# Performance work log

Measured on AMD Instinct MI355X. Metric: run time of the kernel, lower is better.

The kernel has to match this reference:

```python
import jax, jax.numpy as jnp
import numpy as np

HEADS = 8
DIM_HEAD = 64


def setup_inputs() -> dict:
    key = jax.random.key(0)
    ks = jax.random.split(key, 10)
    B, NQ, NK, D, INNER = 4, 2048, 2048, 1024, HEADS * DIM_HEAD
    w_scale = 0.02
    return {
        "x": jax.random.normal(ks[0], (B, NQ, D), jnp.float32),
        "context": jax.random.normal(ks[1], (B, NK, D), jnp.float32),
        "wq": jax.random.normal(ks[2], (D, INNER), jnp.float32) * w_scale,
        "bq": jax.random.normal(ks[3], (INNER,), jnp.float32) * w_scale,
        "wk": jax.random.normal(ks[4], (D, INNER), jnp.float32) * w_scale,
        "bk": jax.random.normal(ks[5], (INNER,), jnp.float32) * w_scale,
        "wv": jax.random.normal(ks[6], (D, INNER), jnp.float32) * w_scale,
        "bv": jax.random.normal(ks[7], (INNER,), jnp.float32) * w_scale,
        "wo": jax.random.normal(ks[8], (INNER, D), jnp.float32) * w_scale,
        "bo": jax.random.normal(ks[9], (D,), jnp.float32) * w_scale,
    }


def _split_heads(t):
    # [b, n, h*d] -> [b, h, n, d]
    b, n, _ = t.shape
    return t.reshape(b, n, HEADS, DIM_HEAD).transpose(0, 2, 1, 3)


def reference(x, context, wq, bq, wk, bk, wv, bv, wo, bo):
    scale = DIM_HEAD ** -0.5
    q = _split_heads(x @ wq + bq)        # [b, h, nq, d]
    k = _split_heads(context @ wk + bk)  # [b, h, nk, d]
    v = _split_heads(context @ wv + bv)  # [b, h, nk, d]
    sim = jnp.einsum('bhid,bhjd->bhij', q, k) * scale  # full score matrix, as in original
    attn = jax.nn.softmax(sim, axis=-1)
    out = jnp.einsum('bhij,bhjd->bhid', attn, v)       # [b, h, nq, d]
    b, h, n, d = out.shape
    out = out.transpose(0, 2, 1, 3).reshape(b, n, h * d)
    return out @ wo + bo
```

## Files before the change

### kernel.cpp

```cpp
#include <hip/hip_runtime.h>
#include <hip/hip_bf16.h>

typedef __attribute__((ext_vector_type(8))) short short8;
typedef __attribute__((ext_vector_type(4))) float f32x4;

__device__ __forceinline__ short f2bf(float f) {
  union { float f; unsigned u; } x; x.f = f;
  unsigned r = x.u + 0x7fffu + ((x.u >> 16) & 1u);
  return (short)(r >> 16);
}

__device__ __forceinline__ void gload16(const short* g, short* l) {
  __builtin_amdgcn_global_load_lds(
      (const __attribute__((address_space(1))) unsigned*)g,
      (__attribute__((address_space(3))) unsigned*)l, 16, 0, 0);
}

__global__ void cast_bf16_kernel(const float* __restrict__ src,
                                 short* __restrict__ dst, int n) {
  int i = (blockIdx.x * 256 + threadIdx.x) * 4;
  if (i < n) {
    float4 f = *(const float4*)(src + i);
    union { short s[4]; uint2 u; } o;
    o.s[0] = f2bf(f.x); o.s[1] = f2bf(f.y);
    o.s[2] = f2bf(f.z); o.s[3] = f2bf(f.w);
    *(uint2*)(dst + i) = o.u;
  }
}

__global__ __launch_bounds__(256) void transpose_cast_kernel(
    const float* __restrict__ src, short* __restrict__ dst, int R, int C) {
  __shared__ short tile[64][72];
  int tpc = C >> 6;
  int bx = blockIdx.x % tpc, by = blockIdx.x / tpc;
  int r0 = by * 64, c0 = bx * 64;
  int tx = threadIdx.x & 15, ty = threadIdx.x >> 4;
#pragma unroll
  for (int i = 0; i < 4; i++) {
    int r = i * 16 + ty;
    float4 f = *(const float4*)(src + (size_t)(r0 + r) * C + c0 + tx * 4);
    union { short s[4]; uint2 u; } o;
    o.s[0] = f2bf(f.x); o.s[1] = f2bf(f.y);
    o.s[2] = f2bf(f.z); o.s[3] = f2bf(f.w);
    *(uint2*)&tile[r][tx * 4] = o.u;
  }
  __syncthreads();
#pragma unroll
  for (int i = 0; i < 4; i++) {
    int c = i * 16 + ty;
    union { short s[4]; uint2 u; } o;
#pragma unroll
    for (int k = 0; k < 4; k++) o.s[k] = tile[tx * 4 + k][c];
    *(uint2*)(dst + (size_t)(c0 + c) * R + r0 + tx * 4) = o.u;
  }
}

__device__ __forceinline__ void gemm_core(
    const short* __restrict__ A, const short* __restrict__ Bt, int K,
    int mblk, int nblk, short* sA, short* sB, f32x4 (&acc)[4][4]) {
  int tid = threadIdx.x;
  int lane = tid & 63, wave = tid >> 6;
  int quad = lane >> 4, l15 = lane & 15;
  int wm = (wave >> 1) * 64, wn = (wave & 1) * 64;
  int sub = lane >> 3, e8 = lane & 7;
  int swz = (e8 ^ sub) << 3;
  int s0 = (quad ^ (l15 & 7)) << 3;
  const short* Ag = A + (size_t)(mblk + 32 * wave + sub) * K + swz;
  const short* Bg = Bt + (size_t)(nblk + 32 * wave + sub) * K + swz;
  short* Al = sA + 4 * wave * 512;
  short* Bl = sB + 4 * wave * 512;

  for (int k0 = 0; k0 < K; k0 += 64) {
    __syncthreads();
#pragma unroll
    for (int t = 0; t < 4; t++) {
      gload16(Ag + (size_t)(8 * t) * K + k0, Al + t * 512);
      gload16(Bg + (size_t)(8 * t) * K + k0, Bl + t * 512);
    }
    __syncthreads();
#pragma unroll
    for (int h = 0; h < 2; h++) {
      int so = s0 ^ (h << 5);
      short8 af[4], bf[4];
#pragma unroll
      for (int mt = 0; mt < 4; mt++)
        af[mt] = *(const short8*)(&sA[(wm + mt * 16 + l15) * 64 + so]);
#pragma unroll
      for (int nt = 0; nt < 4; nt++)
        bf[nt] = *(const short8*)(&sB[(wn + nt * 16 + l15) * 64 + so]);
#pragma unroll
      for (int mt = 0; mt < 4; mt++)
#pragma unroll
        for (int nt = 0; nt < 4; nt++)
          acc[mt][nt] = __builtin_amdgcn_mfma_f32_16x16x32_bf16(
              af[mt], bf[nt], acc[mt][nt], 0, 0, 0);
    }
  }
}

__global__ __launch_bounds__(256) void gemm_qkv(
    const short* __restrict__ xb, const short* __restrict__ cb,
    const short* __restrict__ wqt, const short* __restrict__ wkt,
    const short* __restrict__ wvt,
    const float* __restrict__ bq, const float* __restrict__ bk,
    const float* __restrict__ bv,
    short* __restrict__ Qb, short* __restrict__ Kb, short* __restrict__ Vt) {
  __shared__ __align__(16) short sA[128 * 64];
  __shared__ __align__(16) short sB[128 * 64];
  int z = blockIdx.z;
  const short* A  = (z == 0) ? xb : cb;
  const short* Bt = (z == 0) ? wqt : (z == 1) ? wkt : wvt;
  const float* bias = (z == 0) ? bq : (z == 1) ? bk : bv;
  short* out = (z == 0) ? Qb : (z == 1) ? Kb : Vt;
  float scale = (z == 0) ? 0.18033688011112042f : 1.0f;
  int mblk = blockIdx.x * 128, nblk = blockIdx.y * 128;
  f32x4 acc[4][4] = {};
  gemm_core(A, Bt, 1024, mblk, nblk, sA, sB, acc);

  int lane = threadIdx.x & 63, wave = threadIdx.x >> 6;
  int quad = lane >> 4, l15 = lane & 15;
  int wm = (wave >> 1) * 64, wn = (wave & 1) * 64;
#pragma unroll
  for (int nt = 0; nt < 4; nt++) {
    int col = nblk + wn + nt * 16 + l15;
    float bias_v = bias[col];
    int h = col >> 6, dh = col & 63;
#pragma unroll
    for (int mt = 0; mt < 4; mt++)
#pragma unroll
      for (int r = 0; r < 4; r++) {
        int row = mblk + wm + mt * 16 + quad * 4 + r;
        float v = (acc[mt][nt][r] + bias_v) * scale;
        int b = row >> 11, n = row & 2047;
        size_t base = ((size_t)(b * 8 + h)) << 17;
        size_t idx = (z == 2) ? base + ((size_t)dh << 11) + n
                              : base + ((size_t)n << 6) + dh;
        out[idx] = f2bf(v);
      }
  }
}

__global__ __launch_bounds__(256) void gemm_out(
    const short* __restrict__ Ob, const short* __restrict__ wot,
    const float* __restrict__ bo, float* __restrict__ out) {
  __shared__ __align__(16) short sA[128 * 64];
  __shared__ __align__(16) short sB[128 * 64];
  int mblk = blockIdx.x * 128, nblk = blockIdx.y * 128;
  f32x4 acc[4][4] = {};
  gemm_core(Ob, wot, 512, mblk, nblk, sA, sB, acc);
  int lane = threadIdx.x & 63, wave = threadIdx.x >> 6;
  int quad = lane >> 4, l15 = lane & 15;
  int wm = (wave >> 1) * 64, wn = (wave & 1) * 64;
#pragma unroll
  for (int nt = 0; nt < 4; nt++) {
    int col = nblk + wn + nt * 16 + l15;
    float bias_v = bo[col];
#pragma unroll
    for (int mt = 0; mt < 4; mt++)
#pragma unroll
      for (int r = 0; r < 4; r++) {
        int row = mblk + wm + mt * 16 + quad * 4 + r;
        out[(size_t)row * 1024 + col] = acc[mt][nt][r] + bias_v;
      }
  }
}

__global__ __launch_bounds__(256, 4) void attn_kernel(
    const short* __restrict__ Qb, const short* __restrict__ Kb,
    const short* __restrict__ Vt, short* __restrict__ Ob) {
  __shared__ __align__(16) short sK[64 * 64];
  __shared__ __align__(16) short sV[64 * 64];
  __shared__ __align__(16) unsigned sP[4][640];
  int tid = threadIdx.x;
  int lane = tid & 63, wave = tid >> 6;
  int quad = lane >> 4, l15 = lane & 15;
  int bh = blockIdx.x & 31, qt = blockIdx.x >> 5;
  const short* Qp = Qb + ((size_t)bh << 17);
  const short* Kp = Kb + ((size_t)bh << 17);
  const short* Vp = Vt + ((size_t)bh << 17);
  int qrow0 = qt * 64 + wave * 16;
  short8 qf0 = *(const short8*)(Qp + (size_t)(qrow0 + l15) * 64 + quad * 8);
  short8 qf1 = *(const short8*)(Qp + (size_t)(qrow0 + l15) * 64 + 32 + quad * 8);

  int jk0 = 2 * wave, jk1 = 2 * wave + 1;
  int sub = lane >> 3;
  int e8  = lane & 7;
  int swz = (e8 ^ sub) << 3;
  const short* kg0 = Kp + (size_t)(8 * jk0 + sub) * 64 + e8 * 8;
  const short* kg1 = Kp + (size_t)(8 * jk1 + sub) * 64 + e8 * 8;
  short* kl0 = &sK[(8 * jk0 + sub) * 64 + swz];
  short* kl1 = &sK[(8 * jk1 + sub) * 64 + swz];
  const short* vg0 = Vp + (size_t)(8 * jk0 + sub) * 2048 + e8 * 8;
  const short* vg1 = Vp + (size_t)(8 * jk1 + sub) * 2048 + e8 * 8;
  short* vl0 = &sV[(8 * jk0 + sub) * 64 + swz];
  short* vl1 = &sV[(8 * jk1 + sub) * 64 + swz];

  int s0 = (quad ^ (l15 & 7)) << 3;
  int s1 = s0 ^ 32;

  f32x4 o[4] = {};
  float lsum = 0.f;
  unsigned* pw = &sP[wave][0];

  uint4 rk0 = *(const uint4*)kg0, rk1 = *(const uint4*)kg1;
  uint4 rv0 = *(const uint4*)vg0, rv1 = *(const uint4*)vg1;

  for (int it = 0; it < 32; ++it) {
    __syncthreads();
    *(uint4*)kl0 = rk0; *(uint4*)kl1 = rk1;
    *(uint4*)vl0 = rv0; *(uint4*)vl1 = rv1;
    if (it < 31) {
      int off = (it + 1) * 64;
      rk0 = *(const uint4*)(kg0 + (size_t)off * 64);
      rk1 = *(const uint4*)(kg1 + (size_t)off * 64);
      rv0 = *(const uint4*)(vg0 + off);
      rv1 = *(const uint4*)(vg1 + off);
    }
    __syncthreads();
    f32x4 st[4];
#pragma unroll
    for (int jt = 0; jt < 4; jt++) {
      short8 k0 = *(const short8*)(&sK[(jt * 16 + l15) * 64 + s0]);
      short8 k1 = *(const short8*)(&sK[(jt * 16 + l15) * 64 + s1]);
      f32x4 zz = {0.f, 0.f, 0.f, 0.f};
      zz = __builtin_amdgcn_mfma_f32_16x16x32_bf16(k0, qf0, zz, 0, 0, 0);
      st[jt] = __builtin_amdgcn_mfma_f32_16x16x32_bf16(k1, qf1, zz, 0, 0, 0);
    }
#pragma unroll
    for (int jt = 0; jt < 4; jt++) {
      float p0 = exp2f(st[jt][0]), p1 = exp2f(st[jt][1]);
      float p2 = exp2f(st[jt][2]), p3 = exp2f(st[jt][3]);
      lsum += (p0 + p1) + (p2 + p3);
      union { __hip_bfloat162 b; unsigned u; } a0, a1;
      a0.b = __float22bfloat162_rn(make_float2(p0, p1));
      a1.b = __float22bfloat162_rn(make_float2(p2, p3));
      int kpair = 8 * jt + 2 * quad;
      pw[(kpair + 0) * 20 + l15] = a0.u;
      pw[(kpair + 1) * 20 + l15] = a1.u;
    }
    union { unsigned u[4]; short8 s; } P0, P1;
#pragma unroll
    for (int c = 0; c < 4; c++) {
      P0.u[c] = pw[(4 * quad + c) * 20 + l15];
      P1.u[c] = pw[(16 + 4 * quad + c) * 20 + l15];
    }
#pragma unroll
    for (int nt = 0; nt < 4; nt++) {
      short8 v0 = *(const short8*)(&sV[(nt * 16 + l15) * 64 + s0]);
      short8 v1 = *(const short8*)(&sV[(nt * 16 + l15) * 64 + s1]);
      o[nt] = __builtin_amdgcn_mfma_f32_16x16x32_bf16(v0, P0.s, o[nt], 0, 0, 0);
      o[nt] = __builtin_amdgcn_mfma_f32_16x16x32_bf16(v1, P1.s, o[nt], 0, 0, 0);
    }
  }
  lsum += __shfl_xor(lsum, 16, 64);
  lsum += __shfl_xor(lsum, 32, 64);
  float inv = 1.0f / lsum;
  int b = bh >> 3, h = bh & 7;
  size_t rowbase = ((size_t)b * 2048 + qrow0 + l15) * 512 + h * 64 + quad * 4;
#pragma unroll
  for (int nt = 0; nt < 4; nt++) {
    union { short s[4]; uint2 u; } pk2;
#pragma unroll
    for (int r = 0; r < 4; r++) pk2.s[r] = f2bf(o[nt][r] * inv);
    *(uint2*)(Ob + rowbase + nt * 16) = pk2.u;
  }
}

extern "C" void kernel_launch(void* const* d_in, const int* in_sizes, int n_in,
                              void* d_out, int out_size, void* d_ws, size_t ws_size,
                              hipStream_t stream) {
  const float* x   = (const float*)d_in[0];
  const float* ctx = (const float*)d_in[1];
  const float* wq  = (const float*)d_in[2];
  const float* bq  = (const float*)d_in[3];
  const float* wk  = (const float*)d_in[4];
  const float* bk  = (const float*)d_in[5];
  const float* wv  = (const float*)d_in[6];
  const float* bv  = (const float*)d_in[7];
  const float* wo  = (const float*)d_in[8];
  const float* bo  = (const float*)d_in[9];
  float* out = (float*)d_out;
  char* ws = (char*)d_ws;

  short* xb  = (short*)(ws);
  short* cb  = (short*)(ws + (16ull << 20));
  short* wqt = (short*)(ws + (32ull << 20));
  short* wkt = (short*)(ws + (33ull << 20));
  short* wvt = (short*)(ws + (34ull << 20));
  short* wot = (short*)(ws + (35ull << 20));
  short* Qb  = (short*)(ws + (36ull << 20));
  short* Kb  = (short*)(ws + (44ull << 20));
  short* Vt  = (short*)(ws + (52ull << 20));
  short* Ob  = (short*)(ws + (60ull << 20));

  cast_bf16_kernel<<<8192, 256, 0, stream>>>(x, xb, 1 << 23);
  cast_bf16_kernel<<<8192, 256, 0, stream>>>(ctx, cb, 1 << 23);
  transpose_cast_kernel<<<128, 256, 0, stream>>>(wq, wqt, 1024, 512);
  transpose_cast_kernel<<<128, 256, 0, stream>>>(wk, wkt, 1024, 512);
  transpose_cast_kernel<<<128, 256, 0, stream>>>(wv, wvt, 1024, 512);
  transpose_cast_kernel<<<128, 256, 0, stream>>>(wo, wot, 512, 1024);
  gemm_qkv<<<dim3(64, 4, 3), 256, 0, stream>>>(xb, cb, wqt, wkt, wvt,
                                               bq, bk, bv, Qb, Kb, Vt);
  attn_kernel<<<1024, 256, 0, stream>>>(Qb, Kb, Vt, Ob);
  gemm_out<<<dim3(64, 8), 256, 0, stream>>>(Ob, wot, bo, out);
}
```

Before: 264.7 us.

## Double-buffer attention K/V, process two query groups per wave, fuse prep kernels

```diff
diff --git a/kernel.cpp b/kernel.cpp
--- a/kernel.cpp
+++ b/kernel.cpp
@@ -3,6 +3,7 @@
 
 typedef __attribute__((ext_vector_type(8))) short short8;
 typedef __attribute__((ext_vector_type(4))) float f32x4;
+typedef __attribute__((ext_vector_type(2))) unsigned uint2u;
 
 __device__ __forceinline__ short f2bf(float f) {
   union { float f; unsigned u; } x; x.f = f;
@@ -16,21 +17,29 @@
       (__attribute__((address_space(3))) unsigned*)l, 16, 0, 0);
 }
 
-__global__ void cast_bf16_kernel(const float* __restrict__ src,
-                                 short* __restrict__ dst, int n) {
+__global__ void cast2_bf16_kernel(const float* __restrict__ a,
+                                  const float* __restrict__ b,
+                                  short* __restrict__ dst) {
   int i = (blockIdx.x * 256 + threadIdx.x) * 4;
-  if (i < n) {
-    float4 f = *(const float4*)(src + i);
-    union { short s[4]; uint2 u; } o;
-    o.s[0] = f2bf(f.x); o.s[1] = f2bf(f.y);
-    o.s[2] = f2bf(f.z); o.s[3] = f2bf(f.w);
-    *(uint2*)(dst + i) = o.u;
-  }
-}
-
-__global__ __launch_bounds__(256) void transpose_cast_kernel(
-    const float* __restrict__ src, short* __restrict__ dst, int R, int C) {
+  const float* s = (i < (1 << 23)) ? a : b;
+  int j = i & ((1 << 23) - 1);
+  float4 f = *(const float4*)(s + j);
+  union { short s[4]; uint2 u; } o;
+  o.s[0] = f2bf(f.x); o.s[1] = f2bf(f.y);
+  o.s[2] = f2bf(f.z); o.s[3] = f2bf(f.w);
+  *(uint2*)(dst + i) = o.u;
+}
+
+__global__ __launch_bounds__(256) void transpose_cast4_kernel(
+    const float* __restrict__ wq, const float* __restrict__ wk,
+    const float* __restrict__ wv, const float* __restrict__ wo,
+    short* __restrict__ wqt, short* __restrict__ wkt,
+    short* __restrict__ wvt, short* __restrict__ wot) {
   __shared__ short tile[64][72];
+  int z = blockIdx.z;
+  const float* src = (z == 0) ? wq : (z == 1) ? wk : (z == 2) ? wv : wo;
+  short* dst = (z == 0) ? wqt : (z == 1) ? wkt : (z == 2) ? wvt : wot;
+  int R = (z < 3) ? 1024 : 512, C = (z < 3) ? 512 : 1024;
   int tpc = C >> 6;
   int bx = blockIdx.x % tpc, by = blockIdx.x / tpc;
   int r0 = by * 64, c0 = bx * 64;
@@ -165,12 +174,11 @@
   }
 }
 
-__global__ __launch_bounds__(256, 4) void attn_kernel(
+__global__ __launch_bounds__(256, 2) void attn_kernel(
     const short* __restrict__ Qb, const short* __restrict__ Kb,
     const short* __restrict__ Vt, short* __restrict__ Ob) {
-  __shared__ __align__(16) short sK[64 * 64];
-  __shared__ __align__(16) short sV[64 * 64];
-  __shared__ __align__(16) unsigned sP[4][640];
+  __shared__ __align__(16) short sK[2 * 64 * 64];
+  __shared__ __align__(16) short sV[2 * 64 * 64];
   int tid = threadIdx.x;
   int lane = tid & 63, wave = tid >> 6;
   int quad = lane >> 4, l15 = lane & 15;
@@ -178,9 +186,15 @@
   const short* Qp = Qb + ((size_t)bh << 17);
   const short* Kp = Kb + ((size_t)bh << 17);
   const short* Vp = Vt + ((size_t)bh << 17);
-  int qrow0 = qt * 64 + wave * 16;
-  short8 qf0 = *(const short8*)(Qp + (size_t)(qrow0 + l15) * 64 + quad * 8);
-  short8 qf1 = *(const short8*)(Qp + (size_t)(qrow0 + l15) * 64 + 32 + quad * 8);
+  int qrow0 = qt * 128 + wave * 32;
+
+  short8 qf[2][2];
+#pragma unroll
+  for (int g = 0; g < 2; g++) {
+    const short* qrow = Qp + (size_t)(qrow0 + g * 16 + l15) * 64;
+    qf[g][0] = *(const short8*)(qrow + quad * 8);
+    qf[g][1] = *(const short8*)(qrow + 32 + quad * 8);
+  }
 
   int jk0 = 2 * wave, jk1 = 2 * wave + 1;
   int sub = lane >> 3;
@@ -188,81 +202,102 @@
   int swz = (e8 ^ sub) << 3;
   const short* kg0 = Kp + (size_t)(8 * jk0 + sub) * 64 + e8 * 8;
   const short* kg1 = Kp + (size_t)(8 * jk1 + sub) * 64 + e8 * 8;
-  short* kl0 = &sK[(8 * jk0 + sub) * 64 + swz];
-  short* kl1 = &sK[(8 * jk1 + sub) * 64 + swz];
   const short* vg0 = Vp + (size_t)(8 * jk0 + sub) * 2048 + e8 * 8;
   const short* vg1 = Vp + (size_t)(8 * jk1 + sub) * 2048 + e8 * 8;
-  short* vl0 = &sV[(8 * jk0 + sub) * 64 + swz];
-  short* vl1 = &sV[(8 * jk1 + sub) * 64 + swz];
+  int kw0 = (8 * jk0 + sub) * 64 + swz;
+  int kw1 = (8 * jk1 + sub) * 64 + swz;
 
   int s0 = (quad ^ (l15 & 7)) << 3;
   int s1 = s0 ^ 32;
 
-  f32x4 o[4] = {};
-  float lsum = 0.f;
-  unsigned* pw = &sP[wave][0];
+  f32x4 o[2][4] = {};
+  float lsum[2] = {0.f, 0.f};
 
   uint4 rk0 = *(const uint4*)kg0, rk1 = *(const uint4*)kg1;
   uint4 rv0 = *(const uint4*)vg0, rv1 = *(const uint4*)vg1;
+  *(uint4*)(sK + kw0) = rk0; *(uint4*)(sK + kw1) = rk1;
+  *(uint4*)(sV + kw0) = rv0; *(uint4*)(sV + kw1) = rv1;
+  rk0 = *(const uint4*)(kg0 + 4096); rk1 = *(const uint4*)(kg1 + 4096);
+  rv0 = *(const uint4*)(vg0 + 64);   rv1 = *(const uint4*)(vg1 + 64);
+  __syncthreads();
 
   for (int it = 0; it < 32; ++it) {
-    __syncthreads();
-    *(uint4*)kl0 = rk0; *(uint4*)kl1 = rk1;
-    *(uint4*)vl0 = rv0; *(uint4*)vl1 = rv1;
+    const short* sKr = sK + (it & 1) * 4096;
+    const short* sVr = sV + (it & 1) * 4096;
     if (it < 31) {
-      int off = (it + 1) * 64;
-      rk0 = *(const uint4*)(kg0 + (size_t)off * 64);
-      rk1 = *(const uint4*)(kg1 + (size_t)off * 64);
-      rv0 = *(const uint4*)(vg0 + off);
-      rv1 = *(const uint4*)(vg1 + off);
-    }
-    __syncthreads();
-    f32x4 st[4];
+      short* sKw = sK + ((it & 1) ^ 1) * 4096;
+      short* sVw = sV + ((it & 1) ^ 1) * 4096;
+      *(uint4*)(sKw + kw0) = rk0; *(uint4*)(sKw + kw1) = rk1;
+      *(uint4*)(sVw + kw0) = rv0; *(uint4*)(sVw + kw1) = rv1;
+      if (it < 30) {
+        size_t ko = (size_t)(it + 2) * 4096, vo = (size_t)(it + 2) * 64;
+        rk0 = *(const uint4*)(kg0 + ko); rk1 = *(const uint4*)(kg1 + ko);
+        rv0 = *(const uint4*)(vg0 + vo); rv1 = *(const uint4*)(vg1 + vo);
+      }
+    }
+    unsigned xp[2][4][2];
 #pragma unroll
     for (int jt = 0; jt < 4; jt++) {
-      short8 k0 = *(const short8*)(&sK[(jt * 16 + l15) * 64 + s0]);
-      short8 k1 = *(const short8*)(&sK[(jt * 16 + l15) * 64 + s1]);
-      f32x4 zz = {0.f, 0.f, 0.f, 0.f};
-      zz = __builtin_amdgcn_mfma_f32_16x16x32_bf16(k0, qf0, zz, 0, 0, 0);
-      st[jt] = __builtin_amdgcn_mfma_f32_16x16x32_bf16(k1, qf1, zz, 0, 0, 0);
-    }
-#pragma unroll
-    for (int jt = 0; jt < 4; jt++) {
-      float p0 = exp2f(st[jt][0]), p1 = exp2f(st[jt][1]);
-      float p2 = exp2f(st[jt][2]), p3 = exp2f(st[jt][3]);
-      lsum += (p0 + p1) + (p2 + p3);
-      union { __hip_bfloat162 b; unsigned u; } a0, a1;
-      a0.b = __float22bfloat162_rn(make_float2(p0, p1));
-      a1.b = __float22bfloat162_rn(make_float2(p2, p3));
-      int kpair = 8 * jt + 2 * quad;
-      pw[(kpair + 0) * 20 + l15] = a0.u;
-      pw[(kpair + 1) * 20 + l15] = a1.u;
-    }
-    union { unsigned u[4]; short8 s; } P0, P1;
-#pragma unroll
-    for (int c = 0; c < 4; c++) {
-      P0.u[c] = pw[(4 * quad + c) * 20 + l15];
-      P1.u[c] = pw[(16 + 4 * quad + c) * 20 + l15];
+      short8 k0 = *(const short8*)(&sKr[(jt * 16 + l15) * 64 + s0]);
+      short8 k1 = *(const short8*)(&sKr[(jt * 16 + l15) * 64 + s1]);
+#pragma unroll
+      for (int g = 0; g < 2; g++) {
+        f32x4 zz = {0.f, 0.f, 0.f, 0.f};
+        zz = __builtin_amdgcn_mfma_f32_16x16x32_bf16(k0, qf[g][0], zz, 0, 0, 0);
+        f32x4 st = __builtin_amdgcn_mfma_f32_16x16x32_bf16(k1, qf[g][1], zz, 0, 0, 0);
+        float p0 = exp2f(st[0]), p1 = exp2f(st[1]);
+        float p2 = exp2f(st[2]), p3 = exp2f(st[3]);
+        lsum[g] += (p0 + p1) + (p2 + p3);
+        union { __hip_bfloat162 b; unsigned u; } a0, a1;
+        a0.b = __float22bfloat162_rn(make_float2(p0, p1));
+        a1.b = __float22bfloat162_rn(make_float2(p2, p3));
+        xp[g][jt][0] = a0.u; xp[g][jt][1] = a1.u;
+      }
+    }
+    short8 pf[2][2];
+#pragma unroll
+    for (int g = 0; g < 2; g++) {
+#pragma unroll
+      for (int hb = 0; hb < 2; hb++) {
+        unsigned x0 = xp[g][2 * hb][0], x1 = xp[g][2 * hb][1];
+        unsigned x2 = xp[g][2 * hb + 1][0], x3 = xp[g][2 * hb + 1][1];
+        uint2u r1 = __builtin_amdgcn_permlane32_swap(x0, x2, false, false);
+        uint2u r2 = __builtin_amdgcn_permlane16_swap(r1[0], r1[1], false, false);
+        uint2u r3 = __builtin_amdgcn_permlane32_swap(x1, x3, false, false);
+        uint2u r4 = __builtin_amdgcn_permlane16_swap(r3[0], r3[1], false, false);
+        union { unsigned u[4]; short8 s; } P;
+        P.u[0] = r2[0]; P.u[1] = r4[0]; P.u[2] = r2[1]; P.u[3] = r4[1];
+        pf[g][hb] = P.s;
+      }
     }
 #pragma unroll
     for (int nt = 0; nt < 4; nt++) {
-      short8 v0 = *(const short8*)(&sV[(nt * 16 + l15) * 64 + s0]);
-      short8 v1 = *(const short8*)(&sV[(nt * 16 + l15) * 64 + s1]);
-      o[nt] = __builtin_amdgcn_mfma_f32_16x16x32_bf16(v0, P0.s, o[nt], 0, 0, 0);
-      o[nt] = __builtin_amdgcn_mfma_f32_16x16x32_bf16(v1, P1.s, o[nt], 0, 0, 0);
-    }
-  }
-  lsum += __shfl_xor(lsum, 16, 64);
-  lsum += __shfl_xor(lsum, 32, 64);
-  float inv = 1.0f / lsum;
+      short8 v0 = *(const short8*)(&sVr[(nt * 16 + l15) * 64 + s0]);
+      short8 v1 = *(const short8*)(&sVr[(nt * 16 + l15) * 64 + s1]);
+#pragma unroll
+      for (int g = 0; g < 2; g++) {
+        o[g][nt] = __builtin_amdgcn_mfma_f32_16x16x32_bf16(v0, pf[g][0], o[g][nt], 0, 0, 0);
+        o[g][nt] = __builtin_amdgcn_mfma_f32_16x16x32_bf16(v1, pf[g][1], o[g][nt], 0, 0, 0);
+      }
+    }
+    if (it < 31) __syncthreads();
+  }
+
   int b = bh >> 3, h = bh & 7;
-  size_t rowbase = ((size_t)b * 2048 + qrow0 + l15) * 512 + h * 64 + quad * 4;
-#pragma unroll
-  for (int nt = 0; nt < 4; nt++) {
-    union { short s[4]; uint2 u; } pk2;
-#pragma unroll
-    for (int r = 0; r < 4; r++) pk2.s[r] = f2bf(o[nt][r] * inv);
-    *(uint2*)(Ob + rowbase + nt * 16) = pk2.u;
+#pragma unroll
+  for (int g = 0; g < 2; g++) {
+    float l = lsum[g];
+    l += __shfl_xor(l, 16, 64);
+    l += __shfl_xor(l, 32, 64);
+    float inv = 1.0f / l;
+    size_t rowbase = ((size_t)b * 2048 + qrow0 + g * 16 + l15) * 512 + h * 64 + quad * 4;
+#pragma unroll
+    for (int nt = 0; nt < 4; nt++) {
+      union { short s[4]; uint2 u; } pk2;
+#pragma unroll
+      for (int r = 0; r < 4; r++) pk2.s[r] = f2bf(o[g][nt][r] * inv);
+      *(uint2*)(Ob + rowbase + nt * 16) = pk2.u;
+    }
   }
 }
 
@@ -293,14 +328,11 @@
   short* Vt  = (short*)(ws + (52ull << 20));
   short* Ob  = (short*)(ws + (60ull << 20));
 
-  cast_bf16_kernel<<<8192, 256, 0, stream>>>(x, xb, 1 << 23);
-  cast_bf16_kernel<<<8192, 256, 0, stream>>>(ctx, cb, 1 << 23);
-  transpose_cast_kernel<<<128, 256, 0, stream>>>(wq, wqt, 1024, 512);
-  transpose_cast_kernel<<<128, 256, 0, stream>>>(wk, wkt, 1024, 512);
-  transpose_cast_kernel<<<128, 256, 0, stream>>>(wv, wvt, 1024, 512);
-  transpose_cast_kernel<<<128, 256, 0, stream>>>(wo, wot, 512, 1024);
+  cast2_bf16_kernel<<<16384, 256, 0, stream>>>(x, ctx, xb);
+  transpose_cast4_kernel<<<dim3(128, 1, 4), 256, 0, stream>>>(
+      wq, wk, wv, wo, wqt, wkt, wvt, wot);
   gemm_qkv<<<dim3(64, 4, 3), 256, 0, stream>>>(xb, cb, wqt, wkt, wvt,
                                                bq, bk, bv, Qb, Kb, Vt);
-  attn_kernel<<<1024, 256, 0, stream>>>(Qb, Kb, Vt, Ob);
+  attn_kernel<<<512, 256, 0, stream>>>(Qb, Kb, Vt, Ob);
   gemm_out<<<dim3(64, 8), 256, 0, stream>>>(Ob, wot, bo, out);
 }
```

New measurement: 248.0 us. 6.3% less time.
